# Performance work log

Hardware: AMD Instinct MI355X
Metric: run time of the kernel (lower is better)

Reference implementation:

```python
import jax, jax.numpy as jnp
import numpy as np

B, N = 2048, 64
D, H = 64, 256
CARD_V, UNIT_V, ENEMY_V, AT_V, SRC_V, MODE_V, TER_V, SITE_V, SKILL_V = 400, 100, 120, 50, 30, 10, 12, 25, 60
STATE_SC, CE_SC, SITE_SC, ME_SC, ACT_SC = 64, 8, 6, 8, 16
L_HAND, L_UNIT, L_CE, L_SK, L_VS, L_ME, L_TGT = 16, 8, 8, 8, 16, 16, 8
STATE_IN = STATE_SC + 6 * D + (D + CE_SC) + (D + SITE_SC) + (D + ME_SC)  # 662
ACT_IN = 7 * D + ACT_SC  # 464


def setup_inputs() -> dict:
    key = jax.random.key(0)
    ks = iter(jax.random.split(key, 64))
    nrm = lambda shape, s=1.0: jax.random.normal(next(ks), shape, jnp.float32) * s
    ri = lambda shape, hi: jax.random.randint(next(ks), shape, 0, hi, jnp.int32)
    return {
        'state_scalars': nrm((B, STATE_SC)),
        'mode_id': ri((B,), MODE_V), 'terrain_id': ri((B,), TER_V), 'site_type_id': ri((B,), SITE_V),
        'hand_ids': ri((B, L_HAND), CARD_V), 'hand_mask': ri((B, L_HAND), 2),
        'unit_ids': ri((B, L_UNIT), UNIT_V), 'unit_mask': ri((B, L_UNIT), 2),
        'combat_enemy_ids': ri((B, L_CE), ENEMY_V), 'combat_enemy_scalars': nrm((B, L_CE, CE_SC)), 'combat_enemy_mask': ri((B, L_CE), 2),
        'skill_ids': ri((B, L_SK), SKILL_V), 'skill_mask': ri((B, L_SK), 2),
        'visible_site_ids': ri((B, L_VS), SITE_V), 'visible_site_scalars': nrm((B, L_VS, SITE_SC)), 'visible_site_mask': ri((B, L_VS), 2),
        'map_enemy_ids': ri((B, L_ME), ENEMY_V), 'map_enemy_scalars': nrm((B, L_ME, ME_SC)), 'map_enemy_mask': ri((B, L_ME), 2),
        'action_ids': ri((B, N, 6), SRC_V),  # SRC_V=30 is min over the 6 id vocabs -> always in range
        'action_scalars': nrm((B, N, ACT_SC)),
        'target_enemy_ids': ri((B, N, L_TGT), ENEMY_V), 'target_mask': ri((B, N, L_TGT), 2),
        'card_emb': nrm((CARD_V, D), 0.05), 'unit_emb': nrm((UNIT_V, D), 0.05), 'enemy_emb': nrm((ENEMY_V, D), 0.05),
        'action_type_emb': nrm((AT_V, D), 0.05), 'source_emb': nrm((SRC_V, D), 0.05), 'mode_emb': nrm((MODE_V, D), 0.05),
        'terrain_emb': nrm((TER_V, D), 0.05), 'site_emb': nrm((SITE_V, D), 0.05), 'skill_emb': nrm((SKILL_V, D), 0.05),
        'map_site_emb': nrm((SITE_V, D), 0.05),
        'W_s': nrm((STATE_IN, H), 0.02), 'b_s': jnp.zeros((H,), jnp.float32),
        'W_a': nrm((ACT_IN, H), 0.02), 'b_a': jnp.zeros((H,), jnp.float32),
        'W1': nrm((2 * H, H), 0.02), 'b1': jnp.zeros((H,), jnp.float32),
        'W2': nrm((H, 1), 0.02), 'b2': jnp.zeros((1,), jnp.float32),
        'W_v': nrm((H, 1), 0.02), 'b_v': jnp.zeros((1,), jnp.float32),
    }


def masked_mean(x, mask):
    # x: [..., L, D'], mask: [..., L] (0/1). Empty list -> zeros (count clamped to 1).
    m = mask.astype(x.dtype)[..., None]
    s = jnp.sum(x * m, axis=-2)
    c = jnp.maximum(jnp.sum(m, axis=-2), 1.0)
    return s / c


def reference(state_scalars, mode_id, terrain_id, site_type_id, hand_ids, hand_mask,
              unit_ids, unit_mask, combat_enemy_ids, combat_enemy_scalars, combat_enemy_mask,
              skill_ids, skill_mask, visible_site_ids, visible_site_scalars, visible_site_mask,
              map_enemy_ids, map_enemy_scalars, map_enemy_mask, action_ids, action_scalars,
              target_enemy_ids, target_mask, card_emb, unit_emb, enemy_emb, action_type_emb,
              source_emb, mode_emb, terrain_emb, site_emb, skill_emb, map_site_emb,
              W_s, b_s, W_a, b_a, W1, b1, W2, b2, W_v, b_v):
    # ---- state encoding (batched version of encode_state) ----
    hand_pool = masked_mean(card_emb[hand_ids], hand_mask)            # [B, D]
    unit_pool = masked_mean(unit_emb[unit_ids], unit_mask)            # [B, D]
    ce = jnp.concatenate([enemy_emb[combat_enemy_ids], combat_enemy_scalars], axis=-1)
    ce_pool = masked_mean(ce, combat_enemy_mask)                      # [B, D+CE_SC]
    skill_pool = masked_mean(skill_emb[skill_ids], skill_mask)        # [B, D]
    vs = jnp.concatenate([map_site_emb[visible_site_ids], visible_site_scalars], axis=-1)
    vs_pool = masked_mean(vs, visible_site_mask)                      # [B, D+SITE_SC]
    me = jnp.concatenate([enemy_emb[map_enemy_ids], map_enemy_scalars], axis=-1)
    me_pool = masked_mean(me, map_enemy_mask)                         # [B, D+ME_SC]
    state_input = jnp.concatenate([
        state_scalars, mode_emb[mode_id], hand_pool, unit_pool,
        terrain_emb[terrain_id], site_emb[site_type_id],
        ce_pool, skill_pool, vs_pool, me_pool], axis=-1)              # [B, 662]
    state_repr = jnp.tanh(state_input @ W_s + b_s)                    # [B, H]
    # ---- action encoding (batched encode_actions) ----
    tgt_pool = masked_mean(enemy_emb[target_enemy_ids], target_mask)  # [B, N, D]
    action_input = jnp.concatenate([
        action_type_emb[action_ids[..., 0]], source_emb[action_ids[..., 1]],
        card_emb[action_ids[..., 2]], unit_emb[action_ids[..., 3]],
        enemy_emb[action_ids[..., 4]], skill_emb[action_ids[..., 5]],
        tgt_pool, action_scalars], axis=-1)                           # [B, N, 464]
    action_reprs = jnp.tanh(action_input @ W_a + b_a)                 # [B, N, H]
    # ---- scoring + value heads ----
    state_b = jnp.broadcast_to(state_repr[:, None, :], (state_repr.shape[0], action_reprs.shape[1], state_repr.shape[1]))
    combined = jnp.concatenate([state_b, action_reprs], axis=-1)      # [B, N, 2H]
    logits = (jnp.tanh(combined @ W1 + b1) @ W2 + b2)[..., 0]         # [B, N]
    value = (state_repr @ W_v + b_v)[..., 0]                          # [B]
    return logits, value
```

## Files before the change

### kernel.cpp

```cpp
#include <hip/hip_runtime.h>
#include <hip/hip_bf16.h>

#define BB 2048
#define NN 64
#define DD 64
#define HH 256
#define L_HAND 16
#define L_UNIT 8
#define L_CE 8
#define L_SK 8
#define L_VS 16
#define L_ME 16
#define L_TGT 8
#define STATE_SC 64
#define CE_SC 8
#define SITE_SC 6
#define ME_SC 8
#define ACT_SC 16
#define STATE_IN 662
#define ACT_IN 464

#define SROWS 2
#define SK 672
#define SSTRIDE 676

typedef __attribute__((ext_vector_type(8))) short short8;
typedef __attribute__((ext_vector_type(4))) float f32x4;

__device__ __forceinline__ float fast_tanh(float x) {
    float e = __expf(2.0f * x);
    return 1.0f - 2.0f * __builtin_amdgcn_rcpf(e + 1.0f);
}
__device__ __forceinline__ short f2bs(float x) {
    __hip_bfloat16 h = __float2bfloat16(x);
    return *reinterpret_cast<short*>(&h);
}
__device__ __forceinline__ float bs2f(short u) {
    union { unsigned int i; float f; } v;
    v.i = ((unsigned int)(unsigned short)u) << 16;
    return v.f;
}
__device__ __forceinline__ void async_copy16(const void* gsrc, void* ldst) {
    __builtin_amdgcn_global_load_lds(
        (const __attribute__((address_space(1))) unsigned int*)gsrc,
        (__attribute__((address_space(3))) unsigned int*)ldst, 16, 0, 0);
}
__device__ __forceinline__ float sum16_dpp(float v) {
    int x;
    x = __builtin_amdgcn_update_dpp(0, __float_as_int(v), 0x111, 0xf, 0xf, true);
    v += __int_as_float(x);
    x = __builtin_amdgcn_update_dpp(0, __float_as_int(v), 0x112, 0xf, 0xf, true);
    v += __int_as_float(x);
    x = __builtin_amdgcn_update_dpp(0, __float_as_int(v), 0x114, 0xf, 0xf, true);
    v += __int_as_float(x);
    x = __builtin_amdgcn_update_dpp(0, __float_as_int(v), 0x118, 0xf, 0xf, true);
    v += __int_as_float(x);
    return v;
}

#define RO_AT    0
#define RO_SRC   50
#define RO_CARD  80
#define RO_UNIT  480
#define RO_ENEMY 580
#define RO_SKILL 700
#define EMB_ROWS 760

#define T0 (480 * 256)
#define T1 (T0 + 256 * 256)
#define T2 (T1 + EMB_ROWS * 64)
#define T3 (T2 + SK * 256)
#define T4 (T3 + 256 * 256)

__global__ __launch_bounds__(256) void pack_kernel(
    const float* __restrict__ W_a, const float* __restrict__ W1,
    const float* __restrict__ W_s,
    const float* __restrict__ at_emb, const float* __restrict__ src_emb,
    const float* __restrict__ card_emb, const float* __restrict__ unit_emb,
    const float* __restrict__ enemy_emb, const float* __restrict__ skill_emb,
    ushort* __restrict__ WaP, ushort* __restrict__ W1bP, ushort* __restrict__ emb16,
    ushort* __restrict__ WsP, ushort* __restrict__ W1aP)
{
    const int idx = blockIdx.x * 256 + threadIdx.x;
    if (idx < T0) {
        const int k = idx >> 8, n = idx & 255;
        const float v = (k < ACT_IN) ? W_a[k * HH + n] : 0.f;
        const int pi = (((k >> 5) * 16 + (n >> 4)) * 64 +
                        ((n & 15) + 16 * ((k >> 3) & 3))) * 8 + (k & 7);
        WaP[pi] = (ushort)f2bs(v);
    } else if (idx < T1) {
        const int j = idx - T0;
        const int k = j >> 8, n = j & 255;
        const float v = W1[(256 + k) * HH + n];
        const int pi = (((k >> 5) * 16 + (n >> 4)) * 64 +
                        ((n & 15) + 16 * ((k >> 3) & 3))) * 8 + (k & 7);
        W1bP[pi] = (ushort)f2bs(v);
    } else if (idx < T2) {
        const int j = idx - T1;
        const int row = j >> 6, d = j & 63;
        float v;
        if      (row < RO_SRC)   v = at_emb[row * 64 + d];
        else if (row < RO_CARD)  v = src_emb[(row - RO_SRC) * 64 + d];
        else if (row < RO_UNIT)  v = card_emb[(row - RO_CARD) * 64 + d];
        else if (row < RO_ENEMY) v = unit_emb[(row - RO_UNIT) * 64 + d];
        else if (row < RO_SKILL) v = enemy_emb[(row - RO_ENEMY) * 64 + d];
        else                     v = skill_emb[(row - RO_SKILL) * 64 + d];
        emb16[j] = (ushort)f2bs(v);
    } else if (idx < T3) {
        const int j = idx - T2;
        const int k = j >> 8, n = j & 255;
        const float v = (k < STATE_IN) ? W_s[k * HH + n] : 0.f;
        const int pi = (((k >> 5) * 16 + (n >> 4)) * 64 +
                        ((n & 15) + 16 * ((k >> 3) & 3))) * 8 + (k & 7);
        WsP[pi] = (ushort)f2bs(v);
    } else if (idx < T4) {
        const int j = idx - T3;
        const int k = j >> 8, n = j & 255;
        const float v = W1[k * HH + n];
        const int pi = (((k >> 5) * 16 + (n >> 4)) * 64 +
                        ((n & 15) + 16 * ((k >> 3) & 3))) * 8 + (k & 7);
        W1aP[pi] = (ushort)f2bs(v);
    }
}

__global__ __launch_bounds__(256) void state_mfma_kernel(
    const float* __restrict__ state_scalars,
    const int* __restrict__ mode_id, const int* __restrict__ terrain_id,
    const int* __restrict__ site_type_id,
    const int* __restrict__ hand_ids, const int* __restrict__ hand_mask,
    const int* __restrict__ unit_ids, const int* __restrict__ unit_mask,
    const int* __restrict__ ce_ids, const float* __restrict__ ce_sc, const int* __restrict__ ce_mask,
    const int* __restrict__ skill_ids, const int* __restrict__ skill_mask,
    const int* __restrict__ vs_ids, const float* __restrict__ vs_sc, const int* __restrict__ vs_mask,
    const int* __restrict__ me_ids, const float* __restrict__ me_sc, const int* __restrict__ me_mask,
    const float* __restrict__ mode_emb, const float* __restrict__ ter_emb,
    const float* __restrict__ site_emb, const float* __restrict__ msite_emb,
    const ushort* __restrict__ emb16,
    const ushort* __restrict__ WsP, const float* __restrict__ b_s,
    const ushort* __restrict__ W1aP,
    const float* __restrict__ W_v, const float* __restrict__ b_v,
    float* __restrict__ s_part, float* __restrict__ out_value)
{
    __shared__ float s_in[SROWS * SSTRIDE];
    __shared__ ushort sA2[8 * 64 * 8];
    __shared__ float red[4][4];

    const int t = threadIdx.x;
    const int b0 = blockIdx.x * SROWS;
    const int w = t >> 6;
    const int lane = t & 63;
    const ushort* card16  = emb16 + RO_CARD  * 64;
    const ushort* unit16  = emb16 + RO_UNIT  * 64;
    const ushort* enemy16 = emb16 + RO_ENEMY * 64;
    const ushort* skill16 = emb16 + RO_SKILL * 64;

    for (int u = t; u < SROWS * 84; u += 256) {
        const int r  = u / 84;
        const int un = u - r * 84;
        const int b  = b0 + r;
        float* dst = s_in + r * SSTRIDE;
        if (un < 8) {
            const int o0 = un * 8;
            const float4 f0 = *(const float4*)(state_scalars + b * STATE_SC + o0);
            const float4 f1 = *(const float4*)(state_scalars + b * STATE_SC + o0 + 4);
            *(float4*)(dst + o0) = f0; *(float4*)(dst + o0 + 4) = f1;
        } else if (un < 16) {
            const int d0 = (un - 8) * 8;
            const float4 f0 = *(const float4*)(mode_emb + mode_id[b] * DD + d0);
            const float4 f1 = *(const float4*)(mode_emb + mode_id[b] * DD + d0 + 4);
            *(float4*)(dst + 64 + d0) = f0; *(float4*)(dst + 64 + d0 + 4) = f1;
        } else if (un < 24) {
            const int d0 = (un - 16) * 8;
            float acc[8] = {0,0,0,0,0,0,0,0}; int c = 0;
#pragma unroll
            for (int l = 0; l < L_HAND; ++l) {
                const int mk = hand_mask[b * L_HAND + l]; c += mk;
                const float fm = (float)mk;
                const short8 e = *(const short8*)(card16 + hand_ids[b * L_HAND + l] * 64 + d0);
#pragma unroll
                for (int q = 0; q < 8; ++q) acc[q] = fmaf(fm, bs2f(e[q]), acc[q]);
            }
            const float inv = 1.0f / (float)(c > 1 ? c : 1);
#pragma unroll
            for (int q = 0; q < 8; ++q) dst[128 + d0 + q] = acc[q] * inv;
        } else if (un < 32) {
            const int d0 = (un - 24) * 8;
            float acc[8] = {0,0,0,0,0,0,0,0}; int c = 0;
#pragma unroll
            for (int l = 0; l < L_UNIT; ++l) {
                const int mk = unit_mask[b * L_UNIT + l]; c += mk;
                const float fm = (float)mk;
                const short8 e = *(const short8*)(unit16 + unit_ids[b * L_UNIT + l] * 64 + d0);
#pragma unroll
                for (int q = 0; q < 8; ++q) acc[q] = fmaf(fm, bs2f(e[q]), acc[q]);
            }
            const float inv = 1.0f / (float)(c > 1 ? c : 1);
#pragma unroll
            for (int q = 0; q < 8; ++q) dst[192 + d0 + q] = acc[q] * inv;
        } else if (un < 40) {
            const int d0 = (un - 32) * 8;
            const float4 f0 = *(const float4*)(ter_emb + terrain_id[b] * DD + d0);
            const float4 f1 = *(const float4*)(ter_emb + terrain_id[b] * DD + d0 + 4);
            *(float4*)(dst + 256 + d0) = f0; *(float4*)(dst + 256 + d0 + 4) = f1;
        } else if (un < 48) {
            const int d0 = (un - 40) * 8;
            const float4 f0 = *(const float4*)(site_emb + site_type_id[b] * DD + d0);
            const float4 f1 = *(const float4*)(site_emb + site_type_id[b] * DD + d0 + 4);
            *(float4*)(dst + 320 + d0) = f0; *(float4*)(dst + 320 + d0 + 4) = f1;
        } else if (un < 56) {
            const int d0 = (un - 48) * 8;
            float acc[8] = {0,0,0,0,0,0,0,0}; int c = 0;
#pragma unroll
            for (int l = 0; l < L_CE; ++l) {
                const int mk = ce_mask[b * L_CE + l]; c += mk;
                const float fm = (float)mk;
                const short8 e = *(const short8*)(enemy16 + ce_ids[b * L_CE + l] * 64 + d0);
#pragma unroll
                for (int q = 0; q < 8; ++q) acc[q] = fmaf(fm, bs2f(e[q]), acc[q]);
            }
            const float inv = 1.0f / (float)(c > 1 ? c : 1);
#pragma unroll
            for (int q = 0; q < 8; ++q) dst[384 + d0 + q] = acc[q] * inv;
        } else if (un == 56) {
            float acc[8] = {0,0,0,0,0,0,0,0}; int c = 0;
#pragma unroll
            for (int l = 0; l < L_CE; ++l) {
                const int mk = ce_mask[b * L_CE + l]; c += mk;
                const float fm = (float)mk;
                const float4 f0 = *(const float4*)(ce_sc + (b * L_CE + l) * CE_SC);
                const float4 f1 = *(const float4*)(ce_sc + (b * L_CE + l) * CE_SC + 4);
                acc[0] = fmaf(fm, f0.x, acc[0]); acc[1] = fmaf(fm, f0.y, acc[1]);
                acc[2] = fmaf(fm, f0.z, acc[2]); acc[3] = fmaf(fm, f0.w, acc[3]);
                acc[4] = fmaf(fm, f1.x, acc[4]); acc[5] = fmaf(fm, f1.y, acc[5]);
                acc[6] = fmaf(fm, f1.z, acc[6]); acc[7] = fmaf(fm, f1.w, acc[7]);
            }
            const float inv = 1.0f / (float)(c > 1 ? c : 1);
#pragma unroll
            for (int q = 0; q < 8; ++q) dst[448 + q] = acc[q] * inv;
        } else if (un < 65) {
            const int d0 = (un - 57) * 8;
            float acc[8] = {0,0,0,0,0,0,0,0}; int c = 0;
#pragma unroll
            for (int l = 0; l < L_SK; ++l) {
                const int mk = skill_mask[b * L_SK + l]; c += mk;
                const float fm = (float)mk;
                const short8 e = *(const short8*)(skill16 + skill_ids[b * L_SK + l] * 64 + d0);
#pragma unroll
                for (int q = 0; q < 8; ++q) acc[q] = fmaf(fm, bs2f(e[q]), acc[q]);
            }
            const float inv = 1.0f / (float)(c > 1 ? c : 1);
#pragma unroll
            for (int q = 0; q < 8; ++q) dst[456 + d0 + q] = acc[q] * inv;
        } else if (un < 73) {
            const int d0 = (un - 65) * 8;
            float acc[8] = {0,0,0,0,0,0,0,0}; int c = 0;
#pragma unroll
            for (int l = 0; l < L_VS; ++l) {
                const int mk = vs_mask[b * L_VS + l]; c += mk;
                const float fm = (float)mk;
                const float4 f0 = *(const float4*)(msite_emb + vs_ids[b * L_VS + l] * DD + d0);
                const float4 f1 = *(const float4*)(msite_emb + vs_ids[b * L_VS + l] * DD + d0 + 4);
                acc[0] = fmaf(fm, f0.x, acc[0]); acc[1] = fmaf(fm, f0.y, acc[1]);
                acc[2] = fmaf(fm, f0.z, acc[2]); acc[3] = fmaf(fm, f0.w, acc[3]);
                acc[4] = fmaf(fm, f1.x, acc[4]); acc[5] = fmaf(fm, f1.y, acc[5]);
                acc[6] = fmaf(fm, f1.z, acc[6]); acc[7] = fmaf(fm, f1.w, acc[7]);
            }
            const float inv = 1.0f / (float)(c > 1 ? c : 1);
#pragma unroll
            for (int q = 0; q < 8; ++q) dst[520 + d0 + q] = acc[q] * inv;
        } else if (un == 73) {
            float acc[6] = {0,0,0,0,0,0}; int c = 0;
#pragma unroll
            for (int l = 0; l < L_VS; ++l) {
                const int mk = vs_mask[b * L_VS + l]; c += mk;
                const float fm = (float)mk;
                const float* p = vs_sc + (b * L_VS + l) * SITE_SC;
#pragma unroll
                for (int q = 0; q < 6; ++q) acc[q] = fmaf(fm, p[q], acc[q]);
            }
            const float inv = 1.0f / (float)(c > 1 ? c : 1);
#pragma unroll
            for (int q = 0; q < 6; ++q) dst[584 + q] = acc[q] * inv;
        } else if (un < 82) {
            const int d0 = (un - 74) * 8;
            float acc[8] = {0,0,0,0,0,0,0,0}; int c = 0;
#pragma unroll
            for (int l = 0; l < L_ME; ++l) {
                const int mk = me_mask[b * L_ME + l]; c += mk;
                const float fm = (float)mk;
                const short8 e = *(const short8*)(enemy16 + me_ids[b * L_ME + l] * 64 + d0);
#pragma unroll
                for (int q = 0; q < 8; ++q) acc[q] = fmaf(fm, bs2f(e[q]), acc[q]);
            }
            const float inv = 1.0f / (float)(c > 1 ? c : 1);
#pragma unroll
            for (int q = 0; q < 8; ++q) dst[590 + d0 + q] = acc[q] * inv;
        } else if (un == 82) {
            float acc[8] = {0,0,0,0,0,0,0,0}; int c = 0;
#pragma unroll
            for (int l = 0; l < L_ME; ++l) {
                const int mk = me_mask[b * L_ME + l]; c += mk;
                const float fm = (float)mk;
                const float4 f0 = *(const float4*)(me_sc + (b * L_ME + l) * ME_SC);
                const float4 f1 = *(const float4*)(me_sc + (b * L_ME + l) * ME_SC + 4);
                acc[0] = fmaf(fm, f0.x, acc[0]); acc[1] = fmaf(fm, f0.y, acc[1]);
                acc[2] = fmaf(fm, f0.z, acc[2]); acc[3] = fmaf(fm, f0.w, acc[3]);
                acc[4] = fmaf(fm, f1.x, acc[4]); acc[5] = fmaf(fm, f1.y, acc[5]);
                acc[6] = fmaf(fm, f1.z, acc[6]); acc[7] = fmaf(fm, f1.w, acc[7]);
            }
            const float inv = 1.0f / (float)(c > 1 ? c : 1);
#pragma unroll
            for (int q = 0; q < 8; ++q) dst[654 + q] = acc[q] * inv;
        } else {
#pragma unroll
            for (int q = 0; q < 10; ++q) dst[662 + q] = 0.f;
        }
    }
    __syncthreads();

    const short8* Ws8  = (const short8*)WsP;
    const short8* W1a8 = (const short8*)W1aP;
    const f32x4 zero = {0.f, 0.f, 0.f, 0.f};
    const int m15 = lane & 15;
    const int g = lane >> 4;
    const float* arow = s_in + (m15 & (SROWS - 1)) * SSTRIDE;

    f32x4 acc1[4];
#pragma unroll
    for (int nt = 0; nt < 4; ++nt) acc1[nt] = zero;

    for (int kt = 0; kt < 21; ++kt) {
        const int k0 = kt * 32 + 8 * g;
        const float4 v0 = *(const float4*)(arow + k0);
        const float4 v1 = *(const float4*)(arow + k0 + 4);
        short8 a;
        a[0] = f2bs(v0.x); a[1] = f2bs(v0.y); a[2] = f2bs(v0.z); a[3] = f2bs(v0.w);
        a[4] = f2bs(v1.x); a[5] = f2bs(v1.y); a[6] = f2bs(v1.z); a[7] = f2bs(v1.w);
        short8 bfr[4];
#pragma unroll
        for (int nt = 0; nt < 4; ++nt) bfr[nt] = Ws8[(kt * 16 + w * 4 + nt) * 64 + lane];
#pragma unroll
        for (int nt = 0; nt < 4; ++nt)
            acc1[nt] = __builtin_amdgcn_mfma_f32_16x16x32_bf16(a, bfr[nt], acc1[nt], 0, 0, 0);
    }

    float sr[4][4];
    float pv[4] = {0.f, 0.f, 0.f, 0.f};
#pragma unroll
    for (int nt = 0; nt < 4; ++nt) {
        const int n = w * 64 + nt * 16 + m15;
        const float bsn = b_s[n];
        const float wvn = W_v[n];
#pragma unroll
        for (int r = 0; r < 4; ++r) {
            const float sv = fast_tanh(acc1[nt][r] + bsn);
            sr[nt][r] = sv;
            pv[r] = fmaf(sv, wvn, pv[r]);
        }
    }
#pragma unroll
    for (int r = 0; r < SROWS; ++r) {
        float v = pv[r];
        v += __shfl_xor(v, 1);
        v += __shfl_xor(v, 2);
        v += __shfl_xor(v, 4);
        v += __shfl_xor(v, 8);
        if (lane == 0) red[w][r] = v;
    }
    if (g == 0) {
#pragma unroll
        for (int nt = 0; nt < 4; ++nt) {
            const int n = w * 64 + nt * 16 + m15;
            const int kt2 = n >> 5;
            const int lo16 = (n >> 3) & 3;
#pragma unroll
            for (int r = 0; r < 4; ++r) {
                const int pi = (kt2 * 64 + (r + 16 * lo16)) * 8 + (n & 7);
                sA2[pi] = (ushort)f2bs(sr[nt][r]);
            }
        }
    }
    __syncthreads();

    if (t < SROWS) {
        out_value[b0 + t] = red[0][t] + red[1][t] + red[2][t] + red[3][t] + b_v[0];
    }

    const short8* sA2_8 = (const short8*)sA2;
    f32x4 acc2[4];
#pragma unroll
    for (int nt = 0; nt < 4; ++nt) acc2[nt] = zero;
#pragma unroll
    for (int kt = 0; kt < 8; ++kt) {
        const short8 a2 = sA2_8[kt * 64 + lane];
        short8 bfr[4];
#pragma unroll
        for (int nt = 0; nt < 4; ++nt) bfr[nt] = W1a8[(kt * 16 + w * 4 + nt) * 64 + lane];
#pragma unroll
        for (int nt = 0; nt < 4; ++nt)
            acc2[nt] = __builtin_amdgcn_mfma_f32_16x16x32_bf16(a2, bfr[nt], acc2[nt], 0, 0, 0);
    }
    if (g == 0) {
#pragma unroll
        for (int nt = 0; nt < 4; ++nt) {
            const int n = w * 64 + nt * 16 + m15;
#pragma unroll
            for (int r = 0; r < SROWS; ++r)
                s_part[(b0 + r) * HH + n] = acc2[nt][r];
        }
    }
}

__device__ __forceinline__ short8 tail_chunk(
    int k0, int m, int b,
    const int* __restrict__ tgt_ids, const int* __restrict__ tgt_mask,
    const ushort* __restrict__ emb16, const float* __restrict__ action_scalars)
{
    short8 val;
    if (k0 < 448) {
        const int d = k0 - 384;
        const ushort* enemy16 = emb16 + RO_ENEMY * 64;
        const int base = (b * NN + m) * L_TGT;
        const int4 t0v = *(const int4*)(tgt_ids + base);
        const int4 t1v = *(const int4*)(tgt_ids + base + 4);
        const int4 m0v = *(const int4*)(tgt_mask + base);
        const int4 m1v = *(const int4*)(tgt_mask + base + 4);
        const int tid[8] = {t0v.x, t0v.y, t0v.z, t0v.w, t1v.x, t1v.y, t1v.z, t1v.w};
        const int tmk[8] = {m0v.x, m0v.y, m0v.z, m0v.w, m1v.x, m1v.y, m1v.z, m1v.w};
        float accq[8] = {0.f, 0.f, 0.f, 0.f, 0.f, 0.f, 0.f, 0.f};
        int c = 0;
#pragma unroll
        for (int l = 0; l < L_TGT; ++l) {
            const int mk = tmk[l];
            c += mk;
            const float fm = (float)mk;
            const short8 e = *(const short8*)(enemy16 + tid[l] * 64 + d);
#pragma unroll
            for (int q = 0; q < 8; ++q) accq[q] = fmaf(fm, bs2f(e[q]), accq[q]);
        }
        const float inv = 1.0f / (float)(c > 1 ? c : 1);
#pragma unroll
        for (int q = 0; q < 8; ++q) val[q] = f2bs(accq[q] * inv);
    } else if (k0 < 464) {
        const float* sc = action_scalars + (b * NN + m) * ACT_SC + (k0 - 448);
        const float4 f0 = *(const float4*)sc;
        const float4 f1 = *(const float4*)(sc + 4);
        val[0] = f2bs(f0.x); val[1] = f2bs(f0.y); val[2] = f2bs(f0.z); val[3] = f2bs(f0.w);
        val[4] = f2bs(f1.x); val[5] = f2bs(f1.y); val[6] = f2bs(f1.z); val[7] = f2bs(f1.w);
    } else {
#pragma unroll
        for (int q = 0; q < 8; ++q) val[q] = 0;
    }
    return val;
}

__global__ __launch_bounds__(512) void action_mfma_kernel(
    const int* __restrict__ action_ids, const float* __restrict__ action_scalars,
    const int* __restrict__ tgt_ids, const int* __restrict__ tgt_mask,
    const ushort* __restrict__ emb16,
    const ushort* __restrict__ WaP, const float* __restrict__ b_a,
    const ushort* __restrict__ W1bP, const float* __restrict__ b1,
    const float* __restrict__ W2, const float* __restrict__ b2,
    const float* __restrict__ s_part, float* __restrict__ out_logits)
{
    __shared__ ushort sA[9 * 2048];
    __shared__ float red[8][64];
    __shared__ int s_ids[64 * 6];

    const int t = threadIdx.x;
    const int b = blockIdx.x;
    const int w = t >> 6;
    const int lane = t & 63;
    const int m15 = lane & 15;

    const short8* sA8  = (const short8*)sA;
    short8* sA8w = (short8*)sA;
    const short8* Wa8  = (const short8*)WaP;
    const short8* W1b8 = (const short8*)W1bP;
    const f32x4 zero = {0.f, 0.f, 0.f, 0.f};

    short8 bn0 = Wa8[(w * 2 + 0) * 64 + lane];
    short8 bn1 = Wa8[(w * 2 + 1) * 64 + lane];

    for (int i = t; i < 64 * 6; i += 512) s_ids[i] = action_ids[b * (64 * 6) + i];
    __syncthreads();

    const int ROFFS[6] = {RO_AT, RO_SRC, RO_CARD, RO_UNIT, RO_ENEMY, RO_SKILL};

    if (w < 6) {
        const int kt = w;
        const int j = kt >> 1;
        const int roff = ROFFS[j];
        const int koff = (kt & 1) * 32 + (lane >> 4) * 8;
#pragma unroll
        for (int i = 0; i < 4; ++i) {
            const int id = s_ids[(i * 16 + m15) * 6 + j];
            const ushort* src = emb16 + (roff + id) * 64 + koff;
            async_copy16(src, sA + kt * 2048 + i * 512);
        }
    }

    {
        const int m = lane;
        const int mt_b = m >> 4, mrow = m & 15;
        for (int kc = 48 + w; kc < 60; kc += 8) {
            const int k0 = kc << 3;
            const short8 val = tail_chunk(k0, m, b, tgt_ids, tgt_mask, emb16, action_scalars);
            const int ktl = (k0 >> 5) - 6;
            const int lo = kc & 3;
            sA8w[(ktl * 4 + mt_b) * 64 + mrow + 16 * lo] = val;
        }
    }
    __syncthreads();

    float ba[2];
#pragma unroll
    for (int nt = 0; nt < 2; ++nt) ba[nt] = b_a[w * 32 + nt * 16 + m15];

    f32x4 acc[4][2];
#pragma unroll
    for (int i = 0; i < 4; ++i) { acc[i][0] = zero; acc[i][1] = zero; }

#pragma unroll
    for (int kt = 0; kt < 6; ++kt) {
        const short8 b0 = bn0, b1 = bn1;
        const int nkt = (kt < 5) ? kt + 1 : 12;
        bn0 = Wa8[(nkt * 16 + w * 2 + 0) * 64 + lane];
        bn1 = Wa8[(nkt * 16 + w * 2 + 1) * 64 + lane];
        short8 a[4];
#pragma unroll
        for (int mti = 0; mti < 4; ++mti) a[mti] = sA8[(kt * 4 + mti) * 64 + lane];
        __builtin_amdgcn_s_setprio(1);
#pragma unroll
        for (int mti = 0; mti < 4; ++mti) {
            acc[mti][0] = __builtin_amdgcn_mfma_f32_16x16x32_bf16(a[mti], b0, acc[mti][0], 0, 0, 0);
            acc[mti][1] = __builtin_amdgcn_mfma_f32_16x16x32_bf16(a[mti], b1, acc[mti][1], 0, 0, 0);
        }
        __builtin_amdgcn_s_setprio(0);
    }
    __syncthreads();

    if (w < 6) {
        const int kt = 6 + w;
        const int j = kt >> 1;
        const int roff = ROFFS[j];
        const int koff = (kt & 1) * 32 + (lane >> 4) * 8;
#pragma unroll
        for (int i = 0; i < 4; ++i) {
            const int id = s_ids[(i * 16 + m15) * 6 + j];
            const ushort* src = emb16 + (roff + id) * 64 + koff;
            async_copy16(src, sA + (kt - 6) * 2048 + i * 512);
        }
    }

#pragma unroll
    for (int kt = 12; kt < 15; ++kt) {
        const short8 b0 = bn0, b1 = bn1;
        const int nkt = (kt < 14) ? kt + 1 : 6;
        bn0 = Wa8[(nkt * 16 + w * 2 + 0) * 64 + lane];
        bn1 = Wa8[(nkt * 16 + w * 2 + 1) * 64 + lane];
        short8 a[4];
#pragma unroll
        for (int mti = 0; mti < 4; ++mti) a[mti] = sA8[((kt - 6) * 4 + mti) * 64 + lane];
        __builtin_amdgcn_s_setprio(1);
#pragma unroll
        for (int mti = 0; mti < 4; ++mti) {
            acc[mti][0] = __builtin_amdgcn_mfma_f32_16x16x32_bf16(a[mti], b0, acc[mti][0], 0, 0, 0);
            acc[mti][1] = __builtin_amdgcn_mfma_f32_16x16x32_bf16(a[mti], b1, acc[mti][1], 0, 0, 0);
        }
        __builtin_amdgcn_s_setprio(0);
    }
    __syncthreads();

    short8 cn0, cn1;
#pragma unroll
    for (int kt = 6; kt < 12; ++kt) {
        const short8 b0 = bn0, b1 = bn1;
        if (kt < 11) {
            bn0 = Wa8[((kt + 1) * 16 + w * 2 + 0) * 64 + lane];
            bn1 = Wa8[((kt + 1) * 16 + w * 2 + 1) * 64 + lane];
        } else {
            cn0 = W1b8[(w * 2 + 0) * 64 + lane];
            cn1 = W1b8[(w * 2 + 1) * 64 + lane];
        }
        short8 a[4];
#pragma unroll
        for (int mti = 0; mti < 4; ++mti) a[mti] = sA8[((kt - 6) * 4 + mti) * 64 + lane];
        __builtin_amdgcn_s_setprio(1);
#pragma unroll
        for (int mti = 0; mti < 4; ++mti) {
            acc[mti][0] = __builtin_amdgcn_mfma_f32_16x16x32_bf16(a[mti], b0, acc[mti][0], 0, 0, 0);
            acc[mti][1] = __builtin_amdgcn_mfma_f32_16x16x32_bf16(a[mti], b1, acc[mti][1], 0, 0, 0);
        }
        __builtin_amdgcn_s_setprio(0);
    }
    __syncthreads();

#pragma unroll
    for (int mti = 0; mti < 4; ++mti)
#pragma unroll
        for (int nt = 0; nt < 2; ++nt) {
            const int n = w * 32 + nt * 16 + m15;
            const int kt2 = n >> 5;
            const int lo16 = (n >> 3) & 3;
#pragma unroll
            for (int r = 0; r < 4; ++r) {
                const int mm = mti * 16 + (lane >> 4) * 4 + r;
                const float h = fast_tanh(acc[mti][nt][r] + ba[nt]);
                const int pi = ((kt2 * 4 + mti) * 64 + ((mm & 15) + 16 * lo16)) * 8 + (n & 7);
                sA[pi] = (ushort)f2bs(h);
            }
        }
    __syncthreads();

    float sp[2], w2v[2];
#pragma unroll
    for (int nt = 0; nt < 2; ++nt) {
        const int n = w * 32 + nt * 16 + m15;
        sp[nt]  = s_part[b * HH + n] + b1[n];
        w2v[nt] = W2[n];
    }

#pragma unroll
    for (int i = 0; i < 4; ++i) { acc[i][0] = zero; acc[i][1] = zero; }

#pragma unroll
    for (int kt = 0; kt < 8; ++kt) {
        const short8 b0 = cn0, b1 = cn1;
        if (kt < 7) {
            cn0 = W1b8[((kt + 1) * 16 + w * 2 + 0) * 64 + lane];
            cn1 = W1b8[((kt + 1) * 16 + w * 2 + 1) * 64 + lane];
        }
        short8 a[4];
#pragma unroll
        for (int mti = 0; mti < 4; ++mti) a[mti] = sA8[(kt * 4 + mti) * 64 + lane];
        __builtin_amdgcn_s_setprio(1);
#pragma unroll
        for (int mti = 0; mti < 4; ++mti) {
            acc[mti][0] = __builtin_amdgcn_mfma_f32_16x16x32_bf16(a[mti], b0, acc[mti][0], 0, 0, 0);
            acc[mti][1] = __builtin_amdgcn_mfma_f32_16x16x32_bf16(a[mti], b1, acc[mti][1], 0, 0, 0);
        }
        __builtin_amdgcn_s_setprio(0);
    }

    float part[4][4];
#pragma unroll
    for (int mti = 0; mti < 4; ++mti)
#pragma unroll
        for (int r = 0; r < 4; ++r) part[mti][r] = 0.f;

#pragma unroll
    for (int mti = 0; mti < 4; ++mti)
#pragma unroll
        for (int nt = 0; nt < 2; ++nt)
#pragma unroll
            for (int r = 0; r < 4; ++r)
                part[mti][r] += fast_tanh(acc[mti][nt][r] + sp[nt]) * w2v[nt];

#pragma unroll
    for (int mti = 0; mti < 4; ++mti)
#pragma unroll
        for (int r = 0; r < 4; ++r)
            part[mti][r] = sum16_dpp(part[mti][r]);

    if (m15 == 15) {
#pragma unroll
        for (int mti = 0; mti < 4; ++mti)
#pragma unroll
            for (int r = 0; r < 4; ++r) {
                const int mm = mti * 16 + (lane >> 4) * 4 + r;
                red[w][mm] = part[mti][r];
            }
    }
    __syncthreads();
    if (t < 64) {
        float s = b2[0];
#pragma unroll
        for (int wi = 0; wi < 8; ++wi) s += red[wi][t];
        out_logits[b * NN + t] = s;
    }
}

extern "C" void kernel_launch(void* const* d_in, const int* in_sizes, int n_in,
                              void* d_out, int out_size, void* d_ws, size_t ws_size,
                              hipStream_t stream) {
    const float* state_scalars = (const float*)d_in[0];
    const int*   mode_id       = (const int*)d_in[1];
    const int*   terrain_id    = (const int*)d_in[2];
    const int*   site_type_id  = (const int*)d_in[3];
    const int*   hand_ids      = (const int*)d_in[4];
    const int*   hand_mask     = (const int*)d_in[5];
    const int*   unit_ids      = (const int*)d_in[6];
    const int*   unit_mask     = (const int*)d_in[7];
    const int*   ce_ids        = (const int*)d_in[8];
    const float* ce_sc         = (const float*)d_in[9];
    const int*   ce_mask       = (const int*)d_in[10];
    const int*   skill_ids     = (const int*)d_in[11];
    const int*   skill_mask    = (const int*)d_in[12];
    const int*   vs_ids        = (const int*)d_in[13];
    const float* vs_sc         = (const float*)d_in[14];
    const int*   vs_mask       = (const int*)d_in[15];
    const int*   me_ids        = (const int*)d_in[16];
    const float* me_sc         = (const float*)d_in[17];
    const int*   me_mask       = (const int*)d_in[18];
    const int*   action_ids    = (const int*)d_in[19];
    const float* action_scalars= (const float*)d_in[20];
    const int*   tgt_ids       = (const int*)d_in[21];
    const int*   tgt_mask      = (const int*)d_in[22];
    const float* card_emb      = (const float*)d_in[23];
    const float* unit_emb      = (const float*)d_in[24];
    const float* enemy_emb     = (const float*)d_in[25];
    const float* at_emb        = (const float*)d_in[26];
    const float* src_emb       = (const float*)d_in[27];
    const float* mode_emb      = (const float*)d_in[28];
    const float* ter_emb       = (const float*)d_in[29];
    const float* site_emb      = (const float*)d_in[30];
    const float* skill_emb     = (const float*)d_in[31];
    const float* msite_emb     = (const float*)d_in[32];
    const float* W_s           = (const float*)d_in[33];
    const float* b_s           = (const float*)d_in[34];
    const float* W_a           = (const float*)d_in[35];
    const float* b_a           = (const float*)d_in[36];
    const float* W1            = (const float*)d_in[37];
    const float* b1            = (const float*)d_in[38];
    const float* W2            = (const float*)d_in[39];
    const float* b2            = (const float*)d_in[40];
    const float* W_v           = (const float*)d_in[41];
    const float* b_v           = (const float*)d_in[42];

    float* out_logits = (float*)d_out;
    float* out_value  = (float*)d_out + (size_t)BB * NN;

    char* ws = (char*)d_ws;
    float*  s_part = (float*)ws;
    ushort* WaP    = (ushort*)(ws + 2097152);
    ushort* W1bP   = (ushort*)(ws + 2342912);
    ushort* emb16  = (ushort*)(ws + 2473984);
    ushort* WsP    = (ushort*)(ws + 2571264);
    ushort* W1aP   = (ushort*)(ws + 2915328);

    pack_kernel<<<(T4 + 255) / 256, 256, 0, stream>>>(
        W_a, W1, W_s, at_emb, src_emb, card_emb, unit_emb, enemy_emb, skill_emb,
        WaP, W1bP, emb16, WsP, W1aP);

    state_mfma_kernel<<<BB / SROWS, 256, 0, stream>>>(
        state_scalars, mode_id, terrain_id, site_type_id,
        hand_ids, hand_mask, unit_ids, unit_mask,
        ce_ids, ce_sc, ce_mask, skill_ids, skill_mask,
        vs_ids, vs_sc, vs_mask, me_ids, me_sc, me_mask,
        mode_emb, ter_emb, site_emb, msite_emb, emb16,
        WsP, b_s, W1aP, W_v, b_v, s_part, out_value);

    action_mfma_kernel<<<BB, 512, 0, stream>>>(
        action_ids, action_scalars, tgt_ids, tgt_mask,
        emb16, WaP, b_a, W1bP, b1, W2, b2, s_part, out_logits);
}
```

Measured before the change: 111.1 us.

## Halve action kernel block to 4 waves, each computing 64 output columns

The action kernel now runs 256 threads (4 waves) per batch row instead of 512. Each wave computes four 16-column N tiles instead of two, so each A fragment read from shared memory feeds twice as many MFMAs. Gather, tail-chunk and reduction work is spread over fewer waves to match. The aim is less LDS A-read traffic per FLOP and fewer waves per block, at the cost of more accumulator registers per wave and possibly less latency hiding.

Result: no change. 113.1 us (+1.8%).

```diff
diff --git a/kernel.cpp b/kernel.cpp
--- a/kernel.cpp
+++ b/kernel.cpp
@@ -454,7 +454,7 @@
     return val;
 }
 
-__global__ __launch_bounds__(512) void action_mfma_kernel(
+__global__ __launch_bounds__(256) void action_mfma_kernel(
     const int* __restrict__ action_ids, const float* __restrict__ action_scalars,
     const int* __restrict__ tgt_ids, const int* __restrict__ tgt_mask,
     const ushort* __restrict__ emb16,
@@ -464,7 +464,7 @@
     const float* __restrict__ s_part, float* __restrict__ out_logits)
 {
     __shared__ ushort sA[9 * 2048];
-    __shared__ float red[8][64];
+    __shared__ float red[4][64];
     __shared__ int s_ids[64 * 6];
 
     const int t = threadIdx.x;
@@ -479,31 +479,41 @@
     const short8* W1b8 = (const short8*)W1bP;
     const f32x4 zero = {0.f, 0.f, 0.f, 0.f};
 
-    short8 bn0 = Wa8[(w * 2 + 0) * 64 + lane];
-    short8 bn1 = Wa8[(w * 2 + 1) * 64 + lane];
-
-    for (int i = t; i < 64 * 6; i += 512) s_ids[i] = action_ids[b * (64 * 6) + i];
+    short8 bn0 = Wa8[(w * 4 + 0) * 64 + lane];
+    short8 bn1 = Wa8[(w * 4 + 1) * 64 + lane];
+    short8 bn2 = Wa8[(w * 4 + 2) * 64 + lane];
+    short8 bn3 = Wa8[(w * 4 + 3) * 64 + lane];
+
+    for (int i = t; i < 64 * 6; i += 256) s_ids[i] = action_ids[b * (64 * 6) + i];
     __syncthreads();
 
     const int ROFFS[6] = {RO_AT, RO_SRC, RO_CARD, RO_UNIT, RO_ENEMY, RO_SKILL};
 
-    if (w < 6) {
+    {
         const int kt = w;
         const int j = kt >> 1;
-        const int roff = ROFFS[j];
         const int koff = (kt & 1) * 32 + (lane >> 4) * 8;
 #pragma unroll
         for (int i = 0; i < 4; ++i) {
             const int id = s_ids[(i * 16 + m15) * 6 + j];
-            const ushort* src = emb16 + (roff + id) * 64 + koff;
-            async_copy16(src, sA + kt * 2048 + i * 512);
+            async_copy16(emb16 + (ROFFS[j] + id) * 64 + koff, sA + kt * 2048 + i * 512);
+        }
+    }
+    if (w < 2) {
+        const int kt = 4 + w;
+        const int j = kt >> 1;
+        const int koff = (kt & 1) * 32 + (lane >> 4) * 8;
+#pragma unroll
+        for (int i = 0; i < 4; ++i) {
+            const int id = s_ids[(i * 16 + m15) * 6 + j];
+            async_copy16(emb16 + (ROFFS[j] + id) * 64 + koff, sA + kt * 2048 + i * 512);
         }
     }
 
     {
         const int m = lane;
         const int mt_b = m >> 4, mrow = m & 15;
-        for (int kc = 48 + w; kc < 60; kc += 8) {
+        for (int kc = 48 + w; kc < 60; kc += 4) {
             const int k0 = kc << 3;
             const short8 val = tail_chunk(k0, m, b, tgt_ids, tgt_mask, emb16, action_scalars);
             const int ktl = (k0 >> 5) - 6;
@@ -513,75 +523,97 @@
     }
     __syncthreads();
 
-    float ba[2];
-#pragma unroll
-    for (int nt = 0; nt < 2; ++nt) ba[nt] = b_a[w * 32 + nt * 16 + m15];
-
-    f32x4 acc[4][2];
-#pragma unroll
-    for (int i = 0; i < 4; ++i) { acc[i][0] = zero; acc[i][1] = zero; }
+    float ba[4];
+#pragma unroll
+    for (int nt = 0; nt < 4; ++nt) ba[nt] = b_a[w * 64 + nt * 16 + m15];
+
+    f32x4 acc[4][4];
+#pragma unroll
+    for (int i = 0; i < 4; ++i)
+#pragma unroll
+        for (int j = 0; j < 4; ++j) acc[i][j] = zero;
 
 #pragma unroll
     for (int kt = 0; kt < 6; ++kt) {
-        const short8 b0 = bn0, b1 = bn1;
+        const short8 b0 = bn0, b1 = bn1, b2v = bn2, b3 = bn3;
         const int nkt = (kt < 5) ? kt + 1 : 12;
-        bn0 = Wa8[(nkt * 16 + w * 2 + 0) * 64 + lane];
-        bn1 = Wa8[(nkt * 16 + w * 2 + 1) * 64 + lane];
+        bn0 = Wa8[(nkt * 16 + w * 4 + 0) * 64 + lane];
+        bn1 = Wa8[(nkt * 16 + w * 4 + 1) * 64 + lane];
+        bn2 = Wa8[(nkt * 16 + w * 4 + 2) * 64 + lane];
+        bn3 = Wa8[(nkt * 16 + w * 4 + 3) * 64 + lane];
         short8 a[4];
 #pragma unroll
         for (int mti = 0; mti < 4; ++mti) a[mti] = sA8[(kt * 4 + mti) * 64 + lane];
         __builtin_amdgcn_s_setprio(1);
 #pragma unroll
         for (int mti = 0; mti < 4; ++mti) {
-            acc[mti][0] = __builtin_amdgcn_mfma_f32_16x16x32_bf16(a[mti], b0, acc[mti][0], 0, 0, 0);
-            acc[mti][1] = __builtin_amdgcn_mfma_f32_16x16x32_bf16(a[mti], b1, acc[mti][1], 0, 0, 0);
+            acc[mti][0] = __builtin_amdgcn_mfma_f32_16x16x32_bf16(a[mti], b0,  acc[mti][0], 0, 0, 0);
+            acc[mti][1] = __builtin_amdgcn_mfma_f32_16x16x32_bf16(a[mti], b1,  acc[mti][1], 0, 0, 0);
+            acc[mti][2] = __builtin_amdgcn_mfma_f32_16x16x32_bf16(a[mti], b2v, acc[mti][2], 0, 0, 0);
+            acc[mti][3] = __builtin_amdgcn_mfma_f32_16x16x32_bf16(a[mti], b3,  acc[mti][3], 0, 0, 0);
         }
         __builtin_amdgcn_s_setprio(0);
     }
     __syncthreads();
 
-    if (w < 6) {
+    {
         const int kt = 6 + w;
         const int j = kt >> 1;
-        const int roff = ROFFS[j];
         const int koff = (kt & 1) * 32 + (lane >> 4) * 8;
 #pragma unroll
         for (int i = 0; i < 4; ++i) {
             const int id = s_ids[(i * 16 + m15) * 6 + j];
-            const ushort* src = emb16 + (roff + id) * 64 + koff;
-            async_copy16(src, sA + (kt - 6) * 2048 + i * 512);
+            async_copy16(emb16 + (ROFFS[j] + id) * 64 + koff, sA + (kt - 6) * 2048 + i * 512);
+        }
+    }
+    if (w < 2) {
+        const int kt = 10 + w;
+        const int j = kt >> 1;
+        const int koff = (kt & 1) * 32 + (lane >> 4) * 8;
+#pragma unroll
+        for (int i = 0; i < 4; ++i) {
+            const int id = s_ids[(i * 16 + m15) * 6 + j];
+            async_copy16(emb16 + (ROFFS[j] + id) * 64 + koff, sA + (kt - 6) * 2048 + i * 512);
         }
     }
 
 #pragma unroll
     for (int kt = 12; kt < 15; ++kt) {
-        const short8 b0 = bn0, b1 = bn1;
+        const short8 b0 = bn0, b1 = bn1, b2v = bn2, b3 = bn3;
         const int nkt = (kt < 14) ? kt + 1 : 6;
-        bn0 = Wa8[(nkt * 16 + w * 2 + 0) * 64 + lane];
-        bn1 = Wa8[(nkt * 16 + w * 2 + 1) * 64 + lane];
+        bn0 = Wa8[(nkt * 16 + w * 4 + 0) * 64 + lane];
+        bn1 = Wa8[(nkt * 16 + w * 4 + 1) * 64 + lane];
+        bn2 = Wa8[(nkt * 16 + w * 4 + 2) * 64 + lane];
+        bn3 = Wa8[(nkt * 16 + w * 4 + 3) * 64 + lane];
         short8 a[4];
 #pragma unroll
         for (int mti = 0; mti < 4; ++mti) a[mti] = sA8[((kt - 6) * 4 + mti) * 64 + lane];
         __builtin_amdgcn_s_setprio(1);
 #pragma unroll
         for (int mti = 0; mti < 4; ++mti) {
-            acc[mti][0] = __builtin_amdgcn_mfma_f32_16x16x32_bf16(a[mti], b0, acc[mti][0], 0, 0, 0);
-            acc[mti][1] = __builtin_amdgcn_mfma_f32_16x16x32_bf16(a[mti], b1, acc[mti][1], 0, 0, 0);
+            acc[mti][0] = __builtin_amdgcn_mfma_f32_16x16x32_bf16(a[mti], b0,  acc[mti][0], 0, 0, 0);
+            acc[mti][1] = __builtin_amdgcn_mfma_f32_16x16x32_bf16(a[mti], b1,  acc[mti][1], 0, 0, 0);
+            acc[mti][2] = __builtin_amdgcn_mfma_f32_16x16x32_bf16(a[mti], b2v, acc[mti][2], 0, 0, 0);
+            acc[mti][3] = __builtin_amdgcn_mfma_f32_16x16x32_bf16(a[mti], b3,  acc[mti][3], 0, 0, 0);
         }
         __builtin_amdgcn_s_setprio(0);
     }
     __syncthreads();
 
-    short8 cn0, cn1;
+    short8 cn0, cn1, cn2, cn3;
 #pragma unroll
     for (int kt = 6; kt < 12; ++kt) {
-        const short8 b0 = bn0, b1 = bn1;
+        const short8 b0 = bn0, b1 = bn1, b2v = bn2, b3 = bn3;
         if (kt < 11) {
-            bn0 = Wa8[((kt + 1) * 16 + w * 2 + 0) * 64 + lane];
-            bn1 = Wa8[((kt + 1) * 16 + w * 2 + 1) * 64 + lane];
+            bn0 = Wa8[((kt + 1) * 16 + w * 4 + 0) * 64 + lane];
+            bn1 = Wa8[((kt + 1) * 16 + w * 4 + 1) * 64 + lane];
+            bn2 = Wa8[((kt + 1) * 16 + w * 4 + 2) * 64 + lane];
+            bn3 = Wa8[((kt + 1) * 16 + w * 4 + 3) * 64 + lane];
         } else {
-            cn0 = W1b8[(w * 2 + 0) * 64 + lane];
-            cn1 = W1b8[(w * 2 + 1) * 64 + lane];
+            cn0 = W1b8[(w * 4 + 0) * 64 + lane];
+            cn1 = W1b8[(w * 4 + 1) * 64 + lane];
+            cn2 = W1b8[(w * 4 + 2) * 64 + lane];
+            cn3 = W1b8[(w * 4 + 3) * 64 + lane];
         }
         short8 a[4];
 #pragma unroll
@@ -589,8 +621,10 @@
         __builtin_amdgcn_s_setprio(1);
 #pragma unroll
         for (int mti = 0; mti < 4; ++mti) {
-            acc[mti][0] = __builtin_amdgcn_mfma_f32_16x16x32_bf16(a[mti], b0, acc[mti][0], 0, 0, 0);
-            acc[mti][1] = __builtin_amdgcn_mfma_f32_16x16x32_bf16(a[mti], b1, acc[mti][1], 0, 0, 0);
+            acc[mti][0] = __builtin_amdgcn_mfma_f32_16x16x32_bf16(a[mti], b0,  acc[mti][0], 0, 0, 0);
+            acc[mti][1] = __builtin_amdgcn_mfma_f32_16x16x32_bf16(a[mti], b1,  acc[mti][1], 0, 0, 0);
+            acc[mti][2] = __builtin_amdgcn_mfma_f32_16x16x32_bf16(a[mti], b2v, acc[mti][2], 0, 0, 0);
+            acc[mti][3] = __builtin_amdgcn_mfma_f32_16x16x32_bf16(a[mti], b3,  acc[mti][3], 0, 0, 0);
         }
         __builtin_amdgcn_s_setprio(0);
     }
@@ -599,8 +633,8 @@
 #pragma unroll
     for (int mti = 0; mti < 4; ++mti)
 #pragma unroll
-        for (int nt = 0; nt < 2; ++nt) {
-            const int n = w * 32 + nt * 16 + m15;
+        for (int nt = 0; nt < 4; ++nt) {
+            const int n = w * 64 + nt * 16 + m15;
             const int kt2 = n >> 5;
             const int lo16 = (n >> 3) & 3;
 #pragma unroll
@@ -613,23 +647,27 @@
         }
     __syncthreads();
 
-    float sp[2], w2v[2];
-#pragma unroll
-    for (int nt = 0; nt < 2; ++nt) {
-        const int n = w * 32 + nt * 16 + m15;
+    float sp[4], w2v[4];
+#pragma unroll
+    for (int nt = 0; nt < 4; ++nt) {
+        const int n = w * 64 + nt * 16 + m15;
         sp[nt]  = s_part[b * HH + n] + b1[n];
         w2v[nt] = W2[n];
     }
 
 #pragma unroll
-    for (int i = 0; i < 4; ++i) { acc[i][0] = zero; acc[i][1] = zero; }
+    for (int i = 0; i < 4; ++i)
+#pragma unroll
+        for (int j = 0; j < 4; ++j) acc[i][j] = zero;
 
 #pragma unroll
     for (int kt = 0; kt < 8; ++kt) {
-        const short8 b0 = cn0, b1 = cn1;
+        const short8 b0 = cn0, b1 = cn1, b2v = cn2, b3 = cn3;
         if (kt < 7) {
-            cn0 = W1b8[((kt + 1) * 16 + w * 2 + 0) * 64 + lane];
-            cn1 = W1b8[((kt + 1) * 16 + w * 2 + 1) * 64 + lane];
+            cn0 = W1b8[((kt + 1) * 16 + w * 4 + 0) * 64 + lane];
+            cn1 = W1b8[((kt + 1) * 16 + w * 4 + 1) * 64 + lane];
+            cn2 = W1b8[((kt + 1) * 16 + w * 4 + 2) * 64 + lane];
+            cn3 = W1b8[((kt + 1) * 16 + w * 4 + 3) * 64 + lane];
         }
         short8 a[4];
 #pragma unroll
@@ -637,8 +675,10 @@
         __builtin_amdgcn_s_setprio(1);
 #pragma unroll
         for (int mti = 0; mti < 4; ++mti) {
-            acc[mti][0] = __builtin_amdgcn_mfma_f32_16x16x32_bf16(a[mti], b0, acc[mti][0], 0, 0, 0);
-            acc[mti][1] = __builtin_amdgcn_mfma_f32_16x16x32_bf16(a[mti], b1, acc[mti][1], 0, 0, 0);
+            acc[mti][0] = __builtin_amdgcn_mfma_f32_16x16x32_bf16(a[mti], b0,  acc[mti][0], 0, 0, 0);
+            acc[mti][1] = __builtin_amdgcn_mfma_f32_16x16x32_bf16(a[mti], b1,  acc[mti][1], 0, 0, 0);
+            acc[mti][2] = __builtin_amdgcn_mfma_f32_16x16x32_bf16(a[mti], b2v, acc[mti][2], 0, 0, 0);
+            acc[mti][3] = __builtin_amdgcn_mfma_f32_16x16x32_bf16(a[mti], b3,  acc[mti][3], 0, 0, 0);
         }
         __builtin_amdgcn_s_setprio(0);
     }
@@ -652,7 +692,7 @@
 #pragma unroll
     for (int mti = 0; mti < 4; ++mti)
 #pragma unroll
-        for (int nt = 0; nt < 2; ++nt)
+        for (int nt = 0; nt < 4; ++nt)
 #pragma unroll
             for (int r = 0; r < 4; ++r)
                 part[mti][r] += fast_tanh(acc[mti][nt][r] + sp[nt]) * w2v[nt];
@@ -674,10 +714,7 @@
     }
     __syncthreads();
     if (t < 64) {
-        float s = b2[0];
-#pragma unroll
-        for (int wi = 0; wi < 8; ++wi) s += red[wi][t];
-        out_logits[b * NN + t] = s;
+        out_logits[b * NN + t] = red[0][t] + red[1][t] + red[2][t] + red[3][t] + b2[0];
     }
 }
 
@@ -751,7 +788,7 @@
         mode_emb, ter_emb, site_emb, msite_emb, emb16,
         WsP, b_s, W1aP, W_v, b_v, s_part, out_value);
 
-    action_mfma_kernel<<<BB, 512, 0, stream>>>(
+    action_mfma_kernel<<<BB, 256, 0, stream>>>(
         action_ids, action_scalars, tgt_ids, tgt_mask,
         emb16, WaP, b_a, W1bP, b1, W2, b2, s_part, out_logits);
 }
```

## Stage full action input in LDS and deepen weight prefetch to two tiles

Applied to the files above, without the earlier changes.

Grows the shared staging buffer from 9 to 15 k-tiles so every embedding gather and the tail chunk are issued up front. The action GEMM then runs as one 15-tile loop, dropping the split phases and two intermediate barriers. Weight fragments are now double-buffered two tiles ahead, including the first W1 tiles, to hide global load latency. The cost is about 24 KB more LDS per block, which may lower occupancy, plus higher register pressure from the extra prefetch buffers.

Measured after the change: 109.7 us. No clear change (-1.3%).

```diff
diff --git a/kernel.cpp b/kernel.cpp
--- a/kernel.cpp
+++ b/kernel.cpp
@@ -463,7 +463,7 @@
     const float* __restrict__ W2, const float* __restrict__ b2,
     const float* __restrict__ s_part, float* __restrict__ out_logits)
 {
-    __shared__ ushort sA[9 * 2048];
+    __shared__ ushort sA[15 * 2048];
     __shared__ float red[8][64];
     __shared__ int s_ids[64 * 6];
 
@@ -479,24 +479,34 @@
     const short8* W1b8 = (const short8*)W1bP;
     const f32x4 zero = {0.f, 0.f, 0.f, 0.f};
 
-    short8 bn0 = Wa8[(w * 2 + 0) * 64 + lane];
-    short8 bn1 = Wa8[(w * 2 + 1) * 64 + lane];
+    short8 bp00 = Wa8[(0 * 16 + w * 2 + 0) * 64 + lane];
+    short8 bp01 = Wa8[(0 * 16 + w * 2 + 1) * 64 + lane];
+    short8 bp10 = Wa8[(1 * 16 + w * 2 + 0) * 64 + lane];
+    short8 bp11 = Wa8[(1 * 16 + w * 2 + 1) * 64 + lane];
 
     for (int i = t; i < 64 * 6; i += 512) s_ids[i] = action_ids[b * (64 * 6) + i];
     __syncthreads();
 
     const int ROFFS[6] = {RO_AT, RO_SRC, RO_CARD, RO_UNIT, RO_ENEMY, RO_SKILL};
 
-    if (w < 6) {
+    {
         const int kt = w;
         const int j = kt >> 1;
-        const int roff = ROFFS[j];
         const int koff = (kt & 1) * 32 + (lane >> 4) * 8;
 #pragma unroll
         for (int i = 0; i < 4; ++i) {
             const int id = s_ids[(i * 16 + m15) * 6 + j];
-            const ushort* src = emb16 + (roff + id) * 64 + koff;
-            async_copy16(src, sA + kt * 2048 + i * 512);
+            async_copy16(emb16 + (ROFFS[j] + id) * 64 + koff, sA + kt * 2048 + i * 512);
+        }
+    }
+    if (w < 4) {
+        const int kt = 8 + w;
+        const int j = kt >> 1;
+        const int koff = (kt & 1) * 32 + (lane >> 4) * 8;
+#pragma unroll
+        for (int i = 0; i < 4; ++i) {
+            const int id = s_ids[(i * 16 + m15) * 6 + j];
+            async_copy16(emb16 + (ROFFS[j] + id) * 64 + koff, sA + kt * 2048 + i * 512);
         }
     }
 
@@ -506,7 +516,7 @@
         for (int kc = 48 + w; kc < 60; kc += 8) {
             const int k0 = kc << 3;
             const short8 val = tail_chunk(k0, m, b, tgt_ids, tgt_mask, emb16, action_scalars);
-            const int ktl = (k0 >> 5) - 6;
+            const int ktl = k0 >> 5;
             const int lo = kc & 3;
             sA8w[(ktl * 4 + mt_b) * 64 + mrow + 16 * lo] = val;
         }
@@ -522,70 +532,28 @@
     for (int i = 0; i < 4; ++i) { acc[i][0] = zero; acc[i][1] = zero; }
 
 #pragma unroll
-    for (int kt = 0; kt < 6; ++kt) {
-        const short8 b0 = bn0, b1 = bn1;
-        const int nkt = (kt < 5) ? kt + 1 : 12;
-        bn0 = Wa8[(nkt * 16 + w * 2 + 0) * 64 + lane];
-        bn1 = Wa8[(nkt * 16 + w * 2 + 1) * 64 + lane];
+    for (int kt = 0; kt < 15; ++kt) {
+        short8 b0, b1;
+        if ((kt & 1) == 0) { b0 = bp00; b1 = bp01; }
+        else               { b0 = bp10; b1 = bp11; }
+        if (kt + 2 < 15) {
+            if ((kt & 1) == 0) {
+                bp00 = Wa8[((kt + 2) * 16 + w * 2 + 0) * 64 + lane];
+                bp01 = Wa8[((kt + 2) * 16 + w * 2 + 1) * 64 + lane];
+            } else {
+                bp10 = Wa8[((kt + 2) * 16 + w * 2 + 0) * 64 + lane];
+                bp11 = Wa8[((kt + 2) * 16 + w * 2 + 1) * 64 + lane];
+            }
+        } else if (kt + 2 == 15) {
+            bp10 = W1b8[(0 * 16 + w * 2 + 0) * 64 + lane];
+            bp11 = W1b8[(0 * 16 + w * 2 + 1) * 64 + lane];
+        } else {
+            bp00 = W1b8[(1 * 16 + w * 2 + 0) * 64 + lane];
+            bp01 = W1b8[(1 * 16 + w * 2 + 1) * 64 + lane];
+        }
         short8 a[4];
 #pragma unroll
         for (int mti = 0; mti < 4; ++mti) a[mti] = sA8[(kt * 4 + mti) * 64 + lane];
-        __builtin_amdgcn_s_setprio(1);
-#pragma unroll
-        for (int mti = 0; mti < 4; ++mti) {
-            acc[mti][0] = __builtin_amdgcn_mfma_f32_16x16x32_bf16(a[mti], b0, acc[mti][0], 0, 0, 0);
-            acc[mti][1] = __builtin_amdgcn_mfma_f32_16x16x32_bf16(a[mti], b1, acc[mti][1], 0, 0, 0);
-        }
-        __builtin_amdgcn_s_setprio(0);
-    }
-    __syncthreads();
-
-    if (w < 6) {
-        const int kt = 6 + w;
-        const int j = kt >> 1;
-        const int roff = ROFFS[j];
-        const int koff = (kt & 1) * 32 + (lane >> 4) * 8;
-#pragma unroll
-        for (int i = 0; i < 4; ++i) {
-            const int id = s_ids[(i * 16 + m15) * 6 + j];
-            const ushort* src = emb16 + (roff + id) * 64 + koff;
-            async_copy16(src, sA + (kt - 6) * 2048 + i * 512);
-        }
-    }
-
-#pragma unroll
-    for (int kt = 12; kt < 15; ++kt) {
-        const short8 b0 = bn0, b1 = bn1;
-        const int nkt = (kt < 14) ? kt + 1 : 6;
-        bn0 = Wa8[(nkt * 16 + w * 2 + 0) * 64 + lane];
-        bn1 = Wa8[(nkt * 16 + w * 2 + 1) * 64 + lane];
-        short8 a[4];
-#pragma unroll
-        for (int mti = 0; mti < 4; ++mti) a[mti] = sA8[((kt - 6) * 4 + mti) * 64 + lane];
-        __builtin_amdgcn_s_setprio(1);
-#pragma unroll
-        for (int mti = 0; mti < 4; ++mti) {
-            acc[mti][0] = __builtin_amdgcn_mfma_f32_16x16x32_bf16(a[mti], b0, acc[mti][0], 0, 0, 0);
-            acc[mti][1] = __builtin_amdgcn_mfma_f32_16x16x32_bf16(a[mti], b1, acc[mti][1], 0, 0, 0);
-        }
-        __builtin_amdgcn_s_setprio(0);
-    }
-    __syncthreads();
-
-    short8 cn0, cn1;
-#pragma unroll
-    for (int kt = 6; kt < 12; ++kt) {
-        const short8 b0 = bn0, b1 = bn1;
-        if (kt < 11) {
-            bn0 = Wa8[((kt + 1) * 16 + w * 2 + 0) * 64 + lane];
-            bn1 = Wa8[((kt + 1) * 16 + w * 2 + 1) * 64 + lane];
-        } else {
-            cn0 = W1b8[(w * 2 + 0) * 64 + lane];
-            cn1 = W1b8[(w * 2 + 1) * 64 + lane];
-        }
-        short8 a[4];
-#pragma unroll
-        for (int mti = 0; mti < 4; ++mti) a[mti] = sA8[((kt - 6) * 4 + mti) * 64 + lane];
         __builtin_amdgcn_s_setprio(1);
 #pragma unroll
         for (int mti = 0; mti < 4; ++mti) {
@@ -626,10 +594,17 @@
 
 #pragma unroll
     for (int kt = 0; kt < 8; ++kt) {
-        const short8 b0 = cn0, b1 = cn1;
-        if (kt < 7) {
-            cn0 = W1b8[((kt + 1) * 16 + w * 2 + 0) * 64 + lane];
-            cn1 = W1b8[((kt + 1) * 16 + w * 2 + 1) * 64 + lane];
+        short8 b0, b1;
+        if ((kt & 1) == 0) { b0 = bp10; b1 = bp11; }
+        else               { b0 = bp00; b1 = bp01; }
+        if (kt + 2 < 8) {
+            if ((kt & 1) == 0) {
+                bp10 = W1b8[((kt + 2) * 16 + w * 2 + 0) * 64 + lane];
+                bp11 = W1b8[((kt + 2) * 16 + w * 2 + 1) * 64 + lane];
+            } else {
+                bp00 = W1b8[((kt + 2) * 16 + w * 2 + 0) * 64 + lane];
+                bp01 = W1b8[((kt + 2) * 16 + w * 2 + 1) * 64 + lane];
+            }
         }
         short8 a[4];
 #pragma unroll
```
